# Kernel optimization log

Measured on AMD Instinct MI355X. Metric: run time of the kernel, lower is better.

## Reference

```python
import jax, jax.numpy as jnp
import numpy as np
import math

B, S, D, H = 8, 1024, 512, 8
DH = D // H
SCALE_BASE = 512


def _xpos(x, downscale):
    # x: [B, H, S, DH]; xpos rotary with exponential scale (jamie-stirling RetNet impl)
    s = x.shape[-2]
    d = x.shape[-1]
    half = d // 2
    sv = (jnp.arange(0, d, 2, dtype=jnp.float32) + 0.4 * d) / (1.4 * d)      # [half]
    power = jnp.arange(s, dtype=jnp.float32) / SCALE_BASE
    scale = sv[None, :] ** power[:, None]                                     # [s, half]
    inv_freq = 1.0 / (10000.0 ** (jnp.arange(half, dtype=jnp.float32) / half))
    ang = jnp.arange(s, dtype=jnp.float32)[:, None] * inv_freq[None, :]       # [s, half]
    if downscale:
        scale = 1.0 / scale
    sin = jnp.repeat(jnp.sin(ang) * scale, 2, axis=-1)                        # [s, d]
    cos = jnp.repeat(jnp.cos(ang) * scale, 2, axis=-1)
    rot = jnp.stack((-x[..., 1::2], x[..., ::2]), axis=-1).reshape(x.shape)   # rotate_every_two
    return x * cos + rot * sin


def setup_inputs() -> dict:
    key = jax.random.key(0)
    ks = jax.random.split(key, 7)
    X = jax.random.normal(ks[0], (B, S, D), dtype=jnp.float32)
    # per-head projections stacked: torch init randn/hidden_size
    W_Q = jax.random.normal(ks[1], (H, D, DH), dtype=jnp.float32) / D
    W_K = jax.random.normal(ks[2], (H, D, DH), dtype=jnp.float32) / D
    W_V = jax.random.normal(ks[3], (H, D, DH), dtype=jnp.float32) / D
    W_G = jax.random.normal(ks[4], (D, D), dtype=jnp.float32) / D
    W_O = jax.random.normal(ks[5], (D, D), dtype=jnp.float32) / D
    gn_weight = jnp.ones((D,), dtype=jnp.float32)
    gn_bias = jnp.zeros((D,), dtype=jnp.float32)
    return {"X": X, "W_Q": W_Q, "W_K": W_K, "W_V": W_V, "W_G": W_G,
            "W_O": W_O, "gn_weight": gn_weight, "gn_bias": gn_bias}


def reference(X, W_Q, W_K, W_V, W_G, W_O, gn_weight, gn_bias):
    b, s, _ = X.shape
    # per-head decay gammas and symmetric (non-causal) decay matrix D
    gammas = 1.0 - jnp.exp(jnp.linspace(math.log(1.0 / 32), math.log(1.0 / 512), H)).astype(jnp.float32)
    n = jnp.arange(s)
    Dmat = gammas[:, None, None] ** jnp.abs(n[:, None] - n[None, :]).astype(jnp.float32)  # [H,s,s]
    Q = _xpos(jnp.einsum('bsd,hde->bhse', X, W_Q), False)
    K = _xpos(jnp.einsum('bsd,hde->bhse', X, W_K), True)
    V = jnp.einsum('bsd,hde->bhse', X, W_V)
    scores = jnp.einsum('bhse,bhte->bhst', Q, K)
    p = jax.nn.softmax(scores, axis=-1) * Dmat[None]          # decay-weighted softmax
    Y = jnp.einsum('bhst,bhte->bhse', p, V)                    # [b,H,s,DH]
    Y = jnp.moveaxis(Y, 1, 2).reshape(b, s, H * DH)            # concat heads -> [b,s,D]
    # GroupNorm(H groups) over flattened rows [b*s, D]
    Yg = Y.reshape(-1, H, DH)
    mu = Yg.mean(axis=-1, keepdims=True)
    var = Yg.var(axis=-1, keepdims=True)
    Yn = ((Yg - mu) * jax.lax.rsqrt(var + 1e-5)).reshape(-1, H * DH)
    Yn = (Yn * gn_weight + gn_bias).reshape(b, s, H * DH)
    G = X @ W_G
    swish = G * jax.nn.sigmoid(G)
    return (swish * Yn) @ W_O
```

## Files before the change

### kernel.cpp

```cpp
#include <hip/hip_runtime.h>
#include <math.h>

#define B_ 8
#define S_ 1024
#define D_ 512
#define H_ 8
#define DH_ 64
#define M_ (B_*S_)

typedef __attribute__((ext_vector_type(8))) short short8;
typedef __attribute__((ext_vector_type(4))) short s16x4;
typedef __attribute__((ext_vector_type(4))) float f32x4;
typedef __attribute__((ext_vector_type(4))) unsigned int u32x4;

__device__ inline void tsplit(float x, short& hs, short& ls) {
  unsigned u = __float_as_uint(x);
  hs = (short)(u >> 16);
  float r = x - __uint_as_float(u & 0xFFFF0000u);
  ls = (short)(__float_as_uint(r) >> 16);
}
__device__ inline void splitpack(f32x4 a, f32x4 b, short8& hh, short8& ll) {
  union { u32x4 u; short8 s; } H, L;
#pragma unroll
  for (int j = 0; j < 2; ++j) {
    unsigned u0 = __float_as_uint(a[2 * j]);
    unsigned u1 = __float_as_uint(a[2 * j + 1]);
    H.u[j] = (u0 >> 16) | (u1 & 0xFFFF0000u);
    float r0 = a[2 * j]     - __uint_as_float(u0 & 0xFFFF0000u);
    float r1 = a[2 * j + 1] - __uint_as_float(u1 & 0xFFFF0000u);
    L.u[j] = (__float_as_uint(r0) >> 16) | (__float_as_uint(r1) & 0xFFFF0000u);
    unsigned v0 = __float_as_uint(b[2 * j]);
    unsigned v1 = __float_as_uint(b[2 * j + 1]);
    H.u[2 + j] = (v0 >> 16) | (v1 & 0xFFFF0000u);
    float s0 = b[2 * j]     - __uint_as_float(v0 & 0xFFFF0000u);
    float s1 = b[2 * j + 1] - __uint_as_float(v1 & 0xFFFF0000u);
    L.u[2 + j] = (__float_as_uint(s0) >> 16) | (__float_as_uint(s1) & 0xFFFF0000u);
  }
  hh = H.s; ll = L.s;
}
__device__ inline f32x4 mfma16(short8 a, short8 b, f32x4 c) {
  return __builtin_amdgcn_mfma_f32_16x16x32_bf16(a, b, c, 0, 0, 0);
}
__device__ inline void gload_lds16(const void* g, void* l) {
  __builtin_amdgcn_global_load_lds(
      (const __attribute__((address_space(1))) void*)g,
      (__attribute__((address_space(3))) void*)l, 16, 0, 0);
}


__global__ void xpos_table_kernel(float* __restrict__ tab) {
  int idx = blockIdx.x * 256 + threadIdx.x;
  int s = idx >> 5, i = idx & 31;
  float sv = (2.0f * (float)i + 0.4f * 64.0f) / (1.4f * 64.0f);
  float p = (float)s / 512.0f;
  float scale = powf(sv, p);
  float inv_freq = powf(10000.0f, -((float)i / 32.0f));
  float ang = (float)s * inv_freq;
  float sn = sinf(ang), cs = cosf(ang);
  tab[idx]          = cs * scale;
  tab[32768 + idx]  = sn * scale;
  tab[65536 + idx]  = cs / scale;
  tab[98304 + idx]  = sn / scale;
}

__global__ __launch_bounds__(256) void xsplit_kernel(
    const float* __restrict__ X, short* __restrict__ Xh, short* __restrict__ Xl) {
  const int tid = threadIdx.x;
  const size_t tile = ((size_t)blockIdx.x * 16 + blockIdx.y) * 4096;
#pragma unroll
  for (int i = 0; i < 2; ++i) {
    int idx = tid + i * 256;
    int g = idx >> 6, sl = idx & 63;
    int m = blockIdx.x * 128 + g * 16 + (sl & 15);
    int k = blockIdx.y * 32 + (sl >> 4) * 8;
    const float* xp = X + (size_t)m * 512 + k;
    f32x4 a = *(const f32x4*)xp;
    f32x4 b = *(const f32x4*)(xp + 4);
    short8 hh, ll;
    splitpack(a, b, hh, ll);
    *(short8*)(Xh + tile + (size_t)idx * 8) = hh;
    *(short8*)(Xl + tile + (size_t)idx * 8) = ll;
  }
}

__global__ __launch_bounds__(256) void wprep_kernel(
    const float* __restrict__ Wq, const float* __restrict__ Wk,
    const float* __restrict__ Wv, const float* __restrict__ Wg,
    short* __restrict__ BTh, short* __restrict__ BTl, int gonly) {
  __shared__ float t[64][65];
  const int n0 = blockIdx.x * 64, k0 = blockIdx.y * 64;
  const int tid = threadIdx.x;
  const float* src;
  int ld;
  if (gonly) {
    src = Wg + (size_t)k0 * 512 + n0; ld = 512;
  } else {
    int w = n0 >> 9, nn = n0 & 511;
    if (w == 3) { src = Wg + (size_t)k0 * 512 + nn; ld = 512; }
    else {
      const float* W = (w == 0) ? Wq : ((w == 1) ? Wk : Wv);
      int h = nn >> 6;
      src = W + (size_t)h * D_ * DH_ + (size_t)k0 * 64; ld = 64;
    }
  }
#pragma unroll
  for (int i = 0; i < 4; ++i) {
    int idx = tid + i * 256;
    int kk = idx >> 4, nl4 = (idx & 15) * 4;
    float4 v = *(const float4*)(src + (size_t)kk * ld + nl4);
    t[kk][nl4] = v.x; t[kk][nl4 + 1] = v.y; t[kk][nl4 + 2] = v.z; t[kk][nl4 + 3] = v.w;
  }
  __syncthreads();
#pragma unroll
  for (int i = 0; i < 2; ++i) {
    int idx = tid + i * 256;
    int nl = idx >> 3, ck = idx & 7;
    short8 hh, ll;
#pragma unroll
    for (int j = 0; j < 8; ++j) {
      short h_, l_;
      tsplit(t[ck * 8 + j][nl], h_, l_);
      hh[j] = h_; ll[j] = l_;
    }
    const int n = n0 + nl, k = k0 + ck * 8;
    const size_t off = ((size_t)((n >> 7) * 16 + (k >> 5))) * 4096
                     + (size_t)((n >> 4) & 7) * 512
                     + (size_t)(((k >> 3) & 3) * 16 + (n & 15)) * 8;
    *(short8*)(BTh + off) = hh;
    *(short8*)(BTl + off) = ll;
  }
}

template<int NSUB, int FUSED>
__global__ __launch_bounds__(256, 2) void gemm_mfma_kernel(
    const short* __restrict__ Ah, const short* __restrict__ Al,
    const short* __restrict__ BTh, const short* __restrict__ BTl,
    const float* __restrict__ tab,
    short* __restrict__ QhO, short* __restrict__ QlO,
    short* __restrict__ KhO, short* __restrict__ KlO,
    short* __restrict__ VhT, short* __restrict__ VlT,
    float* __restrict__ G) {
  constexpr int NT = NSUB * 32;
  constexpr int BSZ = NT * 32;
  __shared__ __align__(16) short AsH[2 * 4096], AsL[2 * 4096];
  __shared__ __align__(16) short BsH[2 * BSZ], BsL[2 * BSZ];
  const int m0 = blockIdx.x * 128, by = blockIdx.y;
  const int tid = threadIdx.x, w = tid >> 6, lane = tid & 63;
  const int lx = lane & 15, quad = lane >> 4;
  const int wr = w >> 1, wc = w & 1;
  f32x4 acc[4][NSUB] = {};

  auto stage = [&](int bsel, int kt) {
    const size_t ta = ((size_t)blockIdx.x * 16 + kt) * 4096 + lane * 8;
    gload_lds16(Ah + ta + (size_t)w * 512,       &AsH[bsel * 4096 + w * 512]);
    gload_lds16(Ah + ta + (size_t)(w + 4) * 512, &AsH[bsel * 4096 + (w + 4) * 512]);
    gload_lds16(Al + ta + (size_t)w * 512,       &AsL[bsel * 4096 + w * 512]);
    gload_lds16(Al + ta + (size_t)(w + 4) * 512, &AsL[bsel * 4096 + (w + 4) * 512]);
    if constexpr (NSUB == 4) {
      const size_t tb = ((size_t)by * 16 + kt) * 4096 + lane * 8;
      gload_lds16(BTh + tb + (size_t)w * 512,       &BsH[bsel * BSZ + w * 512]);
      gload_lds16(BTh + tb + (size_t)(w + 4) * 512, &BsH[bsel * BSZ + (w + 4) * 512]);
      gload_lds16(BTl + tb + (size_t)w * 512,       &BsL[bsel * BSZ + w * 512]);
      gload_lds16(BTl + tb + (size_t)(w + 4) * 512, &BsL[bsel * BSZ + (w + 4) * 512]);
    } else {
      const size_t tb = ((size_t)(by >> 1) * 16 + kt) * 4096
                      + (size_t)(by & 1) * 2048 + lane * 8;
      const short* src = (w < 2) ? BTh : BTl;
      short* dst = (w < 2) ? &BsH[bsel * BSZ] : &BsL[bsel * BSZ];
      const int wq = (w & 1) * 2;
      gload_lds16(src + tb + (size_t)wq * 512,       dst + wq * 512);
      gload_lds16(src + tb + (size_t)(wq + 1) * 512, dst + (wq + 1) * 512);
    }
  };

  stage(0, 0);
  int cur = 0;
  for (int t = 0; t < 16; ++t) {
    asm volatile("s_waitcnt lgkmcnt(0)" ::: "memory");
    __builtin_amdgcn_s_barrier();
    asm volatile("" ::: "memory");
    if (t < 15) {
      stage(cur ^ 1, t + 1);
      if constexpr (NSUB == 4)
        asm volatile("s_waitcnt vmcnt(12)" ::: "memory");
      else
        asm volatile("s_waitcnt vmcnt(6)" ::: "memory");
    } else {
      asm volatile("s_waitcnt vmcnt(0)" ::: "memory");
    }
    __builtin_amdgcn_s_barrier();
    asm volatile("" ::: "memory");

    short8 fah[4], fal[4], fbh[NSUB], fbl[NSUB];
#pragma unroll
    for (int i = 0; i < 4; ++i) {
      fah[i] = *(const short8*)&AsH[cur * 4096 + (wr * 4 + i) * 512 + lane * 8];
      fal[i] = *(const short8*)&AsL[cur * 4096 + (wr * 4 + i) * 512 + lane * 8];
    }
#pragma unroll
    for (int i = 0; i < NSUB; ++i) {
      const int g = (NSUB == 4 ? wc * 4 : wc * 2) + i;
      fbh[i] = *(const short8*)&BsH[cur * BSZ + g * 512 + lane * 8];
      fbl[i] = *(const short8*)&BsL[cur * BSZ + g * 512 + lane * 8];
    }
#pragma unroll
    for (int ms = 0; ms < 4; ++ms)
#pragma unroll
      for (int ns = 0; ns < NSUB; ++ns) {
        f32x4 a = acc[ms][ns];
        a = mfma16(fah[ms], fbh[ns], a);
        a = mfma16(fal[ms], fbh[ns], a);
        a = mfma16(fah[ms], fbl[ns], a);
        acc[ms][ns] = a;
      }
    cur ^= 1;
  }
  if constexpr (FUSED) {
    const int w4 = by >> 2;
    const int ncb = (by & 3) * 128 + wc * 64;
    if (w4 < 2) {
      short* Ph = (w4 == 0) ? QhO : KhO;
      short* Pl = (w4 == 0) ? QlO : KlO;
      const float* ct = tab + (w4 ? 65536 : 0);
      const float* st = tab + (w4 ? 98304 : 32768);
#pragma unroll
      for (int ms = 0; ms < 4; ++ms) {
        const int m = m0 + wr * 64 + ms * 16 + quad * 4;
        const int b = m >> 10, sbase = m & 1023;
#pragma unroll
        for (int ns = 0; ns < 4; ++ns) {
          const int n = ncb + ns * 16 + lx;
          const int h = n >> 6, e = n & 63;
          const int i0 = e >> 1;
          const float sgn = (e & 1) ? 1.0f : -1.0f;
          short* ph = Ph + (((size_t)(b * 8 + h)) * 1024 + sbase) * 64 + e;
          short* pl = Pl + (((size_t)(b * 8 + h)) * 1024 + sbase) * 64 + e;
#pragma unroll
          for (int rg = 0; rg < 4; ++rg) {
            const int s = sbase + rg;
            float v = acc[ms][ns][rg];
            float vp = __shfl_xor(v, 1);
            float o = v * ct[s * 32 + i0] + sgn * vp * st[s * 32 + i0];
            short h_, l_;
            tsplit(o, h_, l_);
            ph[rg * 64] = h_;
            pl[rg * 64] = l_;
          }
        }
      }
    } else if (w4 == 2) {
#pragma unroll
      for (int ms = 0; ms < 4; ++ms) {
        const int m = m0 + wr * 64 + ms * 16 + quad * 4;
        const int b = m >> 10, s = m & 1023;
#pragma unroll
        for (int ns = 0; ns < 4; ++ns) {
          const int n = ncb + ns * 16 + lx;
          const int h = n >> 6, e = n & 63;
          s16x4 hh, ll;
#pragma unroll
          for (int rg = 0; rg < 4; ++rg) {
            short h_, l_;
            tsplit(acc[ms][ns][rg], h_, l_);
            hh[rg] = h_; ll[rg] = l_;
          }
          size_t off = (((size_t)(b * 8 + h)) * 64 + e) * 1024 + s;
          *(s16x4*)(VhT + off) = hh;
          *(s16x4*)(VlT + off) = ll;
        }
      }
    } else {
#pragma unroll
      for (int ms = 0; ms < 4; ++ms) {
        const int m = m0 + wr * 64 + ms * 16 + quad * 4;
#pragma unroll
        for (int ns = 0; ns < 4; ++ns) {
          const int n = ncb + ns * 16 + lx;
#pragma unroll
          for (int rg = 0; rg < 4; ++rg) G[(size_t)(m + rg) * 512 + n] = acc[ms][ns][rg];
        }
      }
    }
  } else {
#pragma unroll
    for (int ms = 0; ms < 4; ++ms) {
      const int m = m0 + wr * 64 + ms * 16 + quad * 4;
#pragma unroll
      for (int ns = 0; ns < NSUB; ++ns) {
        const int n = by * NT + wc * (NSUB * 16) + ns * 16 + lx;
#pragma unroll
        for (int rg = 0; rg < 4; ++rg) G[(size_t)(m + rg) * 512 + n] = acc[ms][ns][rg];
      }
    }
  }
}

__global__ __launch_bounds__(256, 2) void attn_mfma_kernel(
    const short* __restrict__ Qh, const short* __restrict__ Ql,
    const short* __restrict__ Kh, const short* __restrict__ Kl,
    const short* __restrict__ VhT, const short* __restrict__ VlT,
    const float* __restrict__ Gp,
    const float* __restrict__ gnw, const float* __restrict__ gnb,
    short* __restrict__ Zh, short* __restrict__ Zl) {
  __shared__ __align__(16) short KhS[2][4096];
  __shared__ __align__(16) short KlS[2][4096];
  __shared__ __align__(16) short VhS[2][4096];
  __shared__ __align__(16) short VlS[2][4096];
  __shared__ __align__(16) short PhS[4][2048];
  const int bh = blockIdx.x, s0 = blockIdx.y * 128;
  const int b = bh >> 3, h = bh & 7;
  const int tid = threadIdx.x;
  const int w = tid >> 6, lane = tid & 63;
  const int lx = lane & 15, quad = lane >> 4;
  const int s0w = s0 + w * 32;
  const float l0c = -3.4657359027997265f;
  const float l1c = -6.2383246250395075f;
  const float gamma = 1.0f - expf(l0c + (float)h * (l1c - l0c) / 7.0f);
  const float lg2g = log2f(gamma);
  const short* Qbh = Qh + (size_t)bh * S_ * DH_;
  const short* Qbl = Ql + (size_t)bh * S_ * DH_;
  const short* Kbh = Kh + (size_t)bh * S_ * DH_;
  const short* Kbl = Kl + (size_t)bh * S_ * DH_;
  const short* VbH = VhT + (size_t)bh * DH_ * S_;
  const short* VbL = VlT + (size_t)bh * DH_ * S_;

  float cl[4], cr[4], w4g[4], b4g[4];
#pragma unroll
  for (int ns = 0; ns < 4; ++ns) {
    cl[ns] = exp2f(lg2g * (float)(ns * 16 + lx));
    cr[ns] = exp2f(lg2g * (float)(63 - ns * 16 - lx));
    w4g[ns] = gnw[h * DH_ + ns * 16 + lx];
    b4g[ns] = gnb[h * DH_ + ns * 16 + lx];
  }

  short8 qfh[2][2], qfl[2][2];
#pragma unroll
  for (int ms = 0; ms < 2; ++ms)
#pragma unroll
    for (int kc = 0; kc < 2; ++kc) {
      size_t off = (size_t)(s0w + ms * 16 + lx) * DH_ + kc * 32 + quad * 8;
      qfh[ms][kc] = *(const short8*)(Qbh + off);
      qfl[ms][kc] = *(const short8*)(Qbl + off);
    }

  auto stageKV = [&](int bsel, int t0n) {
    const int rsub = lane >> 3;
    const int gsw = (lane & 7) ^ (rsub & 7);
    if (w < 2) {
      const short* src = ((w == 0) ? Kbh : Kbl) + (size_t)(t0n + rsub) * 64 + gsw * 8;
      short* dst = (w == 0) ? &KhS[bsel][0] : &KlS[bsel][0];
#pragma unroll
      for (int i = 0; i < 8; ++i)
        gload_lds16(src + (size_t)i * 8 * 64, dst + i * 512);
    } else {
      const short* src = ((w == 2) ? VbH : VbL) + (size_t)rsub * 1024 + t0n + gsw * 8;
      short* dst = (w == 2) ? &VhS[bsel][0] : &VlS[bsel][0];
#pragma unroll
      for (int i = 0; i < 8; ++i)
        gload_lds16(src + (size_t)i * 8 * 1024, dst + i * 512);
    }
  };

  f32x4 O[2][4] = {};
  float lsum[2][4] = {};

  stageKV(0, 0);
  int cur = 0;
  for (int t = 0; t < 16; ++t) {
    const int t0 = t * 64;
    asm volatile("s_waitcnt lgkmcnt(0)" ::: "memory");
    __builtin_amdgcn_s_barrier();
    asm volatile("" ::: "memory");
    if (t < 15) {
      stageKV(cur ^ 1, t0 + 64);
      asm volatile("s_waitcnt vmcnt(8)" ::: "memory");
    } else {
      asm volatile("s_waitcnt vmcnt(0)" ::: "memory");
    }
    __builtin_amdgcn_s_barrier();
    asm volatile("" ::: "memory");

    f32x4 acc[2][4];
#pragma unroll
    for (int ns = 0; ns < 4; ++ns) {
      const int rowk = ns * 16 + lx, rk = (rowk & 7) << 3;
      const short* Kc0 = &KhS[cur][rowk * 64];
      const short* Kc1 = &KlS[cur][rowk * 64];
      short8 kh0 = *(const short8*)(Kc0 + (((quad) << 3) ^ rk));
      short8 kh1 = *(const short8*)(Kc0 + (((4 | quad) << 3) ^ rk));
      short8 kl0 = *(const short8*)(Kc1 + (((quad) << 3) ^ rk));
      short8 kl1 = *(const short8*)(Kc1 + (((4 | quad) << 3) ^ rk));
#pragma unroll
      for (int ms = 0; ms < 2; ++ms) {
        f32x4 a = {};
        a = mfma16(qfh[ms][0], kh0, a);
        a = mfma16(qfl[ms][0], kh0, a);
        a = mfma16(qfh[ms][0], kl0, a);
        a = mfma16(qfh[ms][1], kh1, a);
        a = mfma16(qfl[ms][1], kh1, a);
        a = mfma16(qfh[ms][1], kl1, a);
        acc[ms][ns] = a;
      }
    }
    const int cse = (t0 + 63 < s0w) ? 0 : ((t0 > s0w + 31) ? 1 : 2);
#pragma unroll
    for (int ms = 0; ms < 2; ++ms)
#pragma unroll
      for (int rg = 0; rg < 4; ++rg) {
        const int rloc = ms * 16 + quad * 4 + rg;
        const int srow = s0w + rloc;
        float pe[4], p[4];
#pragma unroll
        for (int ns = 0; ns < 4; ++ns) pe[ns] = __expf(acc[ms][ns][rg]);
        lsum[ms][rg] += (pe[0] + pe[1]) + (pe[2] + pe[3]);
        if (cse == 0) {
          float rf = exp2f(lg2g * (float)(srow - t0 - 63));
#pragma unroll
          for (int ns = 0; ns < 4; ++ns) p[ns] = pe[ns] * rf * cr[ns];
        } else if (cse == 1) {
          float rf = exp2f(lg2g * (float)(t0 - srow));
#pragma unroll
          for (int ns = 0; ns < 4; ++ns) p[ns] = pe[ns] * rf * cl[ns];
        } else {
#pragma unroll
          for (int ns = 0; ns < 4; ++ns)
            p[ns] = pe[ns] * exp2f(lg2g * fabsf((float)(srow - (t0 + ns * 16 + lx))));
        }
        const int r7s = rloc & 7;
        short* Pw = &PhS[w][rloc * 64 + (lx & 7)];
#pragma unroll
        for (int ns = 0; ns < 4; ++ns)
          Pw[(((ns * 2 + (lx >> 3)) ^ r7s) << 3)] =
              (short)((__float_as_uint(p[ns]) + 0x8000u) >> 16);
      }
    short8 pf[2][2];
#pragma unroll
    for (int ms = 0; ms < 2; ++ms) {
      const int rowp = ms * 16 + lx, rp = (rowp & 7) << 3;
#pragma unroll
      for (int kc = 0; kc < 2; ++kc)
        pf[ms][kc] = *(const short8*)&PhS[w][rowp * 64 + ((((kc * 4 + quad)) << 3) ^ rp)];
    }
#pragma unroll
    for (int ns = 0; ns < 4; ++ns) {
      const int rowv = ns * 16 + lx, rv = (rowv & 7) << 3;
      const short* Vc0 = &VhS[cur][rowv * 64];
      const short* Vc1 = &VlS[cur][rowv * 64];
      short8 vh0 = *(const short8*)(Vc0 + (((quad) << 3) ^ rv));
      short8 vh1 = *(const short8*)(Vc0 + (((4 | quad) << 3) ^ rv));
      short8 vl0 = *(const short8*)(Vc1 + (((quad) << 3) ^ rv));
      short8 vl1 = *(const short8*)(Vc1 + (((4 | quad) << 3) ^ rv));
#pragma unroll
      for (int ms = 0; ms < 2; ++ms) {
        f32x4 o = O[ms][ns];
        o = mfma16(pf[ms][0], vh0, o);
        o = mfma16(pf[ms][0], vl0, o);
        o = mfma16(pf[ms][1], vh1, o);
        o = mfma16(pf[ms][1], vl1, o);
        O[ms][ns] = o;
      }
    }
    cur ^= 1;
  }
#pragma unroll
  for (int ms = 0; ms < 2; ++ms)
#pragma unroll
    for (int rg = 0; rg < 4; ++rg) {
      float s = lsum[ms][rg];
      s += __shfl_xor(s, 1);
      s += __shfl_xor(s, 2);
      s += __shfl_xor(s, 4);
      s += __shfl_xor(s, 8);
      const float inv = 1.0f / s;
      const int srow = s0w + ms * 16 + quad * 4 + rg;
      float y[4];
      float rs = 0.0f;
#pragma unroll
      for (int ns = 0; ns < 4; ++ns) { y[ns] = O[ms][ns][rg] * inv; rs += y[ns]; }
      rs += __shfl_xor(rs, 1);
      rs += __shfl_xor(rs, 2);
      rs += __shfl_xor(rs, 4);
      rs += __shfl_xor(rs, 8);
      const float mu = rs * (1.0f / 64.0f);
      float vv = 0.0f;
#pragma unroll
      for (int ns = 0; ns < 4; ++ns) { float d = y[ns] - mu; vv += d * d; }
      vv += __shfl_xor(vv, 1);
      vv += __shfl_xor(vv, 2);
      vv += __shfl_xor(vv, 4);
      vv += __shfl_xor(vv, 8);
      const float rstd = rsqrtf(vv * (1.0f / 64.0f) + 1e-5f);
      const size_t base = (size_t)(b * S_ + srow) * D_ + h * DH_;
      const int m = b * S_ + srow;
      const size_t zb = ((size_t)((m >> 7) * 16 + h * 2)) * 4096
                      + (size_t)((m >> 4) & 7) * 512 + (size_t)(m & 15) * 8;
#pragma unroll
      for (int ns = 0; ns < 4; ++ns) {
        float g = Gp[base + ns * 16 + lx];
        float sw = g / (1.0f + __expf(-g));
        float z = sw * ((y[ns] - mu) * rstd * w4g[ns] + b4g[ns]);
        short zh_, zl_;
        tsplit(z, zh_, zl_);
        const size_t off = zb + (size_t)(ns >> 1) * 4096
                         + (size_t)(((ns * 2 + (lx >> 3)) & 3) * 128) + (lx & 7);
        Zh[off] = zh_;
        Zl[off] = zl_;
      }
    }
}

extern "C" void kernel_launch(void* const* d_in, const int* in_sizes, int n_in,
                              void* d_out, int out_size, void* d_ws, size_t ws_size,
                              hipStream_t stream) {
  const float* X   = (const float*)d_in[0];
  const float* Wq  = (const float*)d_in[1];
  const float* Wk  = (const float*)d_in[2];
  const float* Wv  = (const float*)d_in[3];
  const float* Wg  = (const float*)d_in[4];
  const float* Wo  = (const float*)d_in[5];
  const float* gnw = (const float*)d_in[6];
  const float* gnb = (const float*)d_in[7];
  float* out = (float*)d_out;
  float* ws  = (float*)d_ws;
  const size_t NB = (size_t)M_ * D_;
  float* R0 = ws;
  float* R1 = ws + NB;
  float* R2 = ws + 2 * NB;
  float* R3 = ws + 3 * NB;
  float* tab = ws + 4 * NB;
  short* BTh = (short*)R3;
  short* BTl = BTh + (size_t)2048 * 512;
  short* Xh  = BTh + (size_t)2 * 2048 * 512;
  short* Xl  = (short*)(tab + 131072);
  short* Qh = (short*)R0;  short* Ql = Qh + NB;
  short* Kh = (short*)R1;  short* Kl = Kh + NB;
  short* VhT = (short*)R2; short* VlT = VhT + NB;
  short* Zh = (short*)R3;  short* Zl = Zh + NB;
  short* BToh = (short*)R1;
  short* BTol = BToh + (size_t)512 * 512;

  wprep_kernel<<<dim3(32, 8), 256, 0, stream>>>(Wq, Wk, Wv, Wg, BTh, BTl, 0);
  xpos_table_kernel<<<128, 256, 0, stream>>>(tab);
  xsplit_kernel<<<dim3(64, 16), 256, 0, stream>>>(X, Xh, Xl);
  gemm_mfma_kernel<4, 1><<<dim3(64, 16), 256, 0, stream>>>(
      Xh, Xl, BTh, BTl, tab, Qh, Ql, Kh, Kl, VhT, VlT, out);
  attn_mfma_kernel<<<dim3(64, 8), 256, 0, stream>>>(
      Qh, Ql, Kh, Kl, VhT, VlT, out, gnw, gnb, Zh, Zl);
  wprep_kernel<<<dim3(8, 8), 256, 0, stream>>>(nullptr, nullptr, nullptr, Wo, BToh, BTol, 1);
  gemm_mfma_kernel<2, 0><<<dim3(64, 8), 256, 0, stream>>>(
      Zh, Zl, BToh, BTol, nullptr, nullptr, nullptr, nullptr, nullptr,
      nullptr, nullptr, out);
}
```

Baseline: 214.9 us.

## Replace double-buffered LDS K/V staging with register prefetch to raise occupancy

The attention kernel drops the two-slot LDS ring of direct global-to-LDS loads. Instead each wave prefetches the next K/V tile into registers during the softmax and PV stages, then writes it to a single LDS buffer after a barrier. Halving the K/V LDS footprint and raising launch bounds to three blocks per CU is meant to increase occupancy and latency hiding. In exchange it adds register pressure (eight short8 staging vectors), an extra barrier per iteration, and explicit LDS store instructions.

```diff
diff --git a/kernel.cpp b/kernel.cpp
--- a/kernel.cpp
+++ b/kernel.cpp
@@ -295,17 +295,17 @@
   }
 }
 
-__global__ __launch_bounds__(256, 2) void attn_mfma_kernel(
+__global__ __launch_bounds__(256, 3) void attn_mfma_kernel(
     const short* __restrict__ Qh, const short* __restrict__ Ql,
     const short* __restrict__ Kh, const short* __restrict__ Kl,
     const short* __restrict__ VhT, const short* __restrict__ VlT,
     const float* __restrict__ Gp,
     const float* __restrict__ gnw, const float* __restrict__ gnb,
     short* __restrict__ Zh, short* __restrict__ Zl) {
-  __shared__ __align__(16) short KhS[2][4096];
-  __shared__ __align__(16) short KlS[2][4096];
-  __shared__ __align__(16) short VhS[2][4096];
-  __shared__ __align__(16) short VlS[2][4096];
+  __shared__ __align__(16) short KhS[4096];
+  __shared__ __align__(16) short KlS[4096];
+  __shared__ __align__(16) short VhS[4096];
+  __shared__ __align__(16) short VlS[4096];
   __shared__ __align__(16) short PhS[4][2048];
   const int bh = blockIdx.x, s0 = blockIdx.y * 128;
   const int b = bh >> 3, h = bh & 7;
@@ -343,49 +343,41 @@
       qfl[ms][kc] = *(const short8*)(Qbl + off);
     }
 
-  auto stageKV = [&](int bsel, int t0n) {
-    const int rsub = lane >> 3;
-    const int gsw = (lane & 7) ^ (rsub & 7);
+  const int rsub = lane >> 3;
+  const int gsw = (lane & 7) ^ rsub;
+  short8 stg[8];
+  auto issueKV = [&](int t0n) {
     if (w < 2) {
       const short* src = ((w == 0) ? Kbh : Kbl) + (size_t)(t0n + rsub) * 64 + gsw * 8;
-      short* dst = (w == 0) ? &KhS[bsel][0] : &KlS[bsel][0];
-#pragma unroll
-      for (int i = 0; i < 8; ++i)
-        gload_lds16(src + (size_t)i * 8 * 64, dst + i * 512);
+#pragma unroll
+      for (int i = 0; i < 8; ++i) stg[i] = *(const short8*)(src + (size_t)i * 512);
     } else {
       const short* src = ((w == 2) ? VbH : VbL) + (size_t)rsub * 1024 + t0n + gsw * 8;
-      short* dst = (w == 2) ? &VhS[bsel][0] : &VlS[bsel][0];
-#pragma unroll
-      for (int i = 0; i < 8; ++i)
-        gload_lds16(src + (size_t)i * 8 * 1024, dst + i * 512);
-    }
+#pragma unroll
+      for (int i = 0; i < 8; ++i) stg[i] = *(const short8*)(src + (size_t)i * 8192);
+    }
+  };
+  auto writeKV = [&]() {
+    short* dst = (w == 0) ? KhS : (w == 1) ? KlS : (w == 2) ? VhS : VlS;
+#pragma unroll
+    for (int i = 0; i < 8; ++i)
+      *(short8*)(dst + (i * 8 + rsub) * 64 + (lane & 7) * 8) = stg[i];
   };
 
   f32x4 O[2][4] = {};
   float lsum[2][4] = {};
 
-  stageKV(0, 0);
-  int cur = 0;
+  issueKV(0);
+  writeKV();
   for (int t = 0; t < 16; ++t) {
     const int t0 = t * 64;
-    asm volatile("s_waitcnt lgkmcnt(0)" ::: "memory");
-    __builtin_amdgcn_s_barrier();
-    asm volatile("" ::: "memory");
-    if (t < 15) {
-      stageKV(cur ^ 1, t0 + 64);
-      asm volatile("s_waitcnt vmcnt(8)" ::: "memory");
-    } else {
-      asm volatile("s_waitcnt vmcnt(0)" ::: "memory");
-    }
-    __builtin_amdgcn_s_barrier();
-    asm volatile("" ::: "memory");
-
+    __syncthreads();
     f32x4 acc[2][4];
 #pragma unroll
     for (int ns = 0; ns < 4; ++ns) {
       const int rowk = ns * 16 + lx, rk = (rowk & 7) << 3;
-      const short* Kc0 = &KhS[cur][rowk * 64];
-      const short* Kc1 = &KlS[cur][rowk * 64];
+      const short* Kc0 = &KhS[rowk * 64];
+      const short* Kc1 = &KlS[rowk * 64];
       short8 kh0 = *(const short8*)(Kc0 + (((quad) << 3) ^ rk));
       short8 kh1 = *(const short8*)(Kc0 + (((4 | quad) << 3) ^ rk));
       short8 kl0 = *(const short8*)(Kc1 + (((quad) << 3) ^ rk));
@@ -402,6 +394,7 @@
         acc[ms][ns] = a;
       }
     }
+    if (t < 15) issueKV(t0 + 64);
     const int cse = (t0 + 63 < s0w) ? 0 : ((t0 > s0w + 31) ? 1 : 2);
 #pragma unroll
     for (int ms = 0; ms < 2; ++ms)
@@ -444,8 +437,8 @@
 #pragma unroll
     for (int ns = 0; ns < 4; ++ns) {
       const int rowv = ns * 16 + lx, rv = (rowv & 7) << 3;
-      const short* Vc0 = &VhS[cur][rowv * 64];
-      const short* Vc1 = &VlS[cur][rowv * 64];
+      const short* Vc0 = &VhS[rowv * 64];
+      const short* Vc1 = &VlS[rowv * 64];
       short8 vh0 = *(const short8*)(Vc0 + (((quad) << 3) ^ rv));
       short8 vh1 = *(const short8*)(Vc0 + (((4 | quad) << 3) ^ rv));
       short8 vl0 = *(const short8*)(Vc1 + (((quad) << 3) ^ rv));
@@ -460,7 +453,8 @@
         O[ms][ns] = o;
       }
     }
-    cur ^= 1;
+    __syncthreads();
+    if (t < 15) writeKV();
   }
 #pragma unroll
   for (int ms = 0; ms < 2; ++ms)
```

New measurement: 469.4 us. 2.18x slower.
